# Kernel optimization log

Measured on AMD Instinct MI355X. Metric: run time of the kernel, lower is better.

Reference implementation:

```python
import jax, jax.numpy as jnp
import numpy as np
import math
from jax import lax

B, T, IN_DIM, D, H, L, OUT = 2, 2048, 128, 512, 8, 4, 128
HD = D // H
FF = int(4.0 * D)
NEG = -1e30  # stands in for -inf in the causal mask (identical softmax result)


def setup_inputs() -> dict:
    key = jax.random.key(0)
    ks = jax.random.split(key, 8)
    s = 0.02
    def p(k, shape):
        return jax.random.normal(k, shape, jnp.float32) * s
    return {
        "x": jax.random.normal(ks[0], (B, T, IN_DIM), jnp.float32),
        "Win": p(ks[1], (IN_DIM, D)), "bin_": jnp.zeros((D,), jnp.float32),
        "Wqkv": p(ks[2], (L, D, 3 * D)), "bqkv": jnp.zeros((L, 3 * D), jnp.float32),
        "Wo": p(ks[3], (L, D, D)), "bo": jnp.zeros((L, D), jnp.float32),
        "ln1_g": jnp.ones((L, D), jnp.float32), "ln1_b": jnp.zeros((L, D), jnp.float32),
        "Wf1": p(ks[4], (L, D, FF)), "bf1": jnp.zeros((L, FF), jnp.float32),
        "Wf2": p(ks[5], (L, FF, D)), "bf2": jnp.zeros((L, D), jnp.float32),
        "ln2_g": jnp.ones((L, D), jnp.float32), "ln2_b": jnp.zeros((L, D), jnp.float32),
        "lnf_g": jnp.ones((D,), jnp.float32), "lnf_b": jnp.zeros((D,), jnp.float32),
        "Wout": p(ks[6], (D, OUT)), "bout": jnp.zeros((OUT,), jnp.float32),
    }


def _layernorm(x, g, b, eps=1e-5):
    mu = jnp.mean(x, axis=-1, keepdims=True)
    var = jnp.mean(jnp.square(x - mu), axis=-1, keepdims=True)
    return (x - mu) * lax.rsqrt(var + eps) * g + b


def _sinusoidal_pe(t, d):
    pos = jnp.arange(t, dtype=jnp.float32)[:, None]
    div = jnp.exp(jnp.arange(0, d, 2, dtype=jnp.float32) * (-math.log(10000.0) / d))
    pe = jnp.zeros((t, d), jnp.float32)
    pe = pe.at[:, 0::2].set(jnp.sin(pos * div)).at[:, 1::2].set(jnp.cos(pos * div))
    return pe


def _alibi_bias():
    # ALiBi slopes (H=8 is a power of 2): start = 2**(-2**(-(log2(H)-3)))
    start = 2.0 ** (-(2.0 ** (-(math.log2(H) - 3.0))))
    slopes = jnp.array([start * (start ** i) for i in range(H)], jnp.float32)
    pos = jnp.arange(T)
    dist = jnp.triu(pos[None, :] - pos[:, None]).astype(jnp.float32)  # faithful: .triu() zeroes j<i
    bias = slopes[:, None, None] * dist  # [H,T,T]
    causal = jnp.triu(jnp.ones((T, T), bool), 1)
    return jnp.where(causal[None], NEG, bias)


def _forward(x, Win, bin_, Wqkv, bqkv, Wo, bo, ln1_g, ln1_b, Wf1, bf1, Wf2, bf2,
             ln2_g, ln2_b, lnf_g, lnf_b, Wout, bout):
    x = x @ Win + bin_                      # [B,T,D] project_in
    x = x + _sinusoidal_pe(T, D)            # internal time embedding
    bias = _alibi_bias()                    # [H,T,T]
    scale = 1.0 / math.sqrt(HD)

    def block(h, params):
        wqkv, bq, wo, bo_, g1, b1, wf1, bf1_, wf2, bf2_, g2, b2 = params
        y = _layernorm(h, g1, b1)
        qkv = y @ wqkv + bq                 # [B,T,3D]
        q, k, v = jnp.split(qkv, 3, axis=-1)
        def heads(t):
            return t.reshape(B, T, H, HD).transpose(0, 2, 1, 3)  # [B,H,T,HD]
        q, k, v = heads(q), heads(k), heads(v)
        logits = jnp.einsum('bhqd,bhkd->bhqk', q, k) * scale + bias[None]
        attn = jax.nn.softmax(logits, axis=-1)
        y = jnp.einsum('bhqk,bhkd->bhqd', attn, v)
        y = y.transpose(0, 2, 1, 3).reshape(B, T, D)
        h = h + (y @ wo + bo_)
        y = _layernorm(h, g2, b2)
        y = jax.nn.gelu(y @ wf1 + bf1_, approximate=False) @ wf2 + bf2_
        h = h + y
        return h, None

    x, _ = lax.scan(block, x, (Wqkv, bqkv, Wo, bo, ln1_g, ln1_b, Wf1, bf1, Wf2, bf2, ln2_g, ln2_b))
    x = _layernorm(x, lnf_g, lnf_b)         # final_norm
    return x @ Wout + bout                  # output head


def reference(x, Win, bin_, Wqkv, bqkv, Wo, bo, ln1_g, ln1_b, Wf1, bf1, Wf2, bf2,
              ln2_g, ln2_b, lnf_g, lnf_b, Wout, bout):
    return _forward(x, Win, bin_, Wqkv, bqkv, Wo, bo, ln1_g, ln1_b, Wf1, bf1,
                    Wf2, bf2, ln2_g, ln2_b, lnf_g, lnf_b, Wout, bout)
```

## Files before the change

kernel.cpp:

```cpp
#include <hip/hip_runtime.h>
#include <math.h>
#include <type_traits>
#include <utility>

#define TT 2048
typedef unsigned short u16;
typedef unsigned int u32;
typedef float f32x4 __attribute__((ext_vector_type(4)));
typedef float f32x16 __attribute__((ext_vector_type(16)));
typedef short s16x8 __attribute__((ext_vector_type(8)));
typedef __bf16 bf16x8 __attribute__((ext_vector_type(8)));
typedef __bf16 bf16x2 __attribute__((ext_vector_type(2)));
typedef u32 u32x4 __attribute__((ext_vector_type(4)));

#define L2E8 0.1803368801111731f
#define EXP2(x) __builtin_amdgcn_exp2f(x)

enum { EPI_PE = 0, EPI_QKV = 1, EPI_RES = 2, EPI_GELU = 3, EPI_OUTF = 4 };

template<typename V, typename = void> struct mfma32_takes : std::false_type {};
template<typename V> struct mfma32_takes<V, std::void_t<decltype(
    __builtin_amdgcn_mfma_f32_32x32x16_bf16(std::declval<V>(), std::declval<V>(),
                                            std::declval<f32x16>(), 0, 0, 0))>>
    : std::true_type {};

template<typename VA>
__device__ __forceinline__ f32x16 MFMA32(VA a, VA b, f32x16 c) {
    if constexpr (mfma32_takes<VA>::value) {
        return __builtin_amdgcn_mfma_f32_32x32x16_bf16(a, b, c, 0, 0, 0);
    } else {
        return __builtin_amdgcn_mfma_f32_32x32x16_bf16(
            __builtin_bit_cast(bf16x8, a), __builtin_bit_cast(bf16x8, b), c, 0, 0, 0);
    }
}

__device__ __forceinline__ u16 f2b(float f) {
    u32 u = __float_as_uint(f);
    return (u16)((u + 0x7FFFu + ((u >> 16) & 1u)) >> 16);
}

__device__ __forceinline__ u32 pkbf(float a, float b) {
    bf16x2 t; t[0] = (__bf16)a; t[1] = (__bf16)b;
    return __builtin_bit_cast(u32, t);
}

__device__ __forceinline__ void gload16(const void* g, void* lds_base, int lds_byte_off) {
    __builtin_amdgcn_global_load_lds(
        (const __attribute__((address_space(1))) void*)g,
        (__attribute__((address_space(3))) void*)((char*)lds_base + lds_byte_off),
        16, 0, 0);
}

template<int EPI, int TM, int TN>
__global__ __launch_bounds__(256)
void k_gemm_mfma(const u16* __restrict__ A, const u16* __restrict__ Bt,
                 const float* __restrict__ bias, const float* __restrict__ Rf,
                 void* __restrict__ Cout, u16* __restrict__ Kfp,
                 u16* __restrict__ Vfp, int M, int N, int K)
{
    constexpr int MF = TM / 64;
    constexpr int NF = TN / 64;
    __shared__ __attribute__((aligned(16))) u16 SMEM[TM * 64 + TN * 64];
    u16* As = SMEM;
    u16* Bs = SMEM + TM * 64;
    const int tid = threadIdx.x;
    const int l = tid & 63, wv = tid >> 6;
    const int l31 = l & 31, hi = l >> 5;
    const int wr = wv >> 1, wc = wv & 1;
    const int row0 = blockIdx.y * TM, col0 = blockIdx.x * TN;

    f32x16 acc[MF][NF] = {};

    for (int kt = 0; kt < K; kt += 64) {
#pragma unroll
        for (int i = 0; i < TM / 32; ++i) {
            const int u = i * 256 + wv * 64 + l;
            const int ar = u >> 3, ac = u & 7;
            const int sc = (ac ^ (ar & 7)) << 3;
            const int off = __builtin_amdgcn_readfirstlane((i * 256 + wv * 64) * 16);
            gload16(A + (size_t)(row0 + ar) * K + kt + sc, As, off);
        }
#pragma unroll
        for (int i = 0; i < TN / 32; ++i) {
            const int u = i * 256 + wv * 64 + l;
            const int ar = u >> 3, ac = u & 7;
            const int sc = (ac ^ (ar & 7)) << 3;
            const int off = __builtin_amdgcn_readfirstlane((i * 256 + wv * 64) * 16);
            gload16(Bt + (size_t)(col0 + ar) * K + kt + sc, Bs, off);
        }
        __syncthreads();
        s16x8 af[MF][4], bf[NF][4];
#pragma unroll
        for (int m = 0; m < MF; ++m) {
            const int r = wr * (TM / 2) + m * 32 + l31;
#pragma unroll
            for (int kk = 0; kk < 4; ++kk)
                af[m][kk] = *(const s16x8*)(As + r * 64 + (((kk * 2 + hi) ^ (r & 7)) << 3));
        }
#pragma unroll
        for (int n = 0; n < NF; ++n) {
            const int r = wc * (TN / 2) + n * 32 + l31;
#pragma unroll
            for (int kk = 0; kk < 4; ++kk)
                bf[n][kk] = *(const s16x8*)(Bs + r * 64 + (((kk * 2 + hi) ^ (r & 7)) << 3));
        }
#pragma unroll
        for (int kk = 0; kk < 4; ++kk)
#pragma unroll
            for (int m = 0; m < MF; ++m)
#pragma unroll
                for (int n = 0; n < NF; ++n)
                    acc[m][n] = MFMA32(af[m][kk], bf[n][kk], acc[m][n]);
        __syncthreads();
    }

    if constexpr (EPI == EPI_QKV) {
        if (col0 < 512) {
#pragma unroll
            for (int m = 0; m < MF; ++m)
#pragma unroll
                for (int r = 0; r < 16; ++r) {
                    const int row = row0 + wr * (TM / 2) + m * 32 + (r & 3) + 8 * (r >> 2) + 4 * hi;
#pragma unroll
                    for (int n = 0; n < NF; ++n) {
                        const int col = col0 + wc * (TN / 2) + n * 32 + l31;
                        ((u16*)Cout)[(size_t)row * N + col] = f2b(acc[m][n][r] + bias[col]);
                    }
                }
        } else if (col0 < 1024) {
#pragma unroll
            for (int m = 0; m < MF; ++m)
#pragma unroll
                for (int r = 0; r < 16; ++r) {
                    const int row = row0 + wr * (TM / 2) + m * 32 + (r & 3) + 8 * (r >> 2) + 4 * hi;
                    const int t = row & (TT - 1), bb = row >> 11;
#pragma unroll
                    for (int n = 0; n < NF; ++n) {
                        const int col = col0 + wc * (TN / 2) + n * 32 + l31;
                        const int dd = col - 512;
                        const int hh = dd >> 6, c = (dd >> 3) & 7, j = dd & 7;
                        Kfp[(((size_t)(bb * 8 + hh) * 8 + c) * 2048 + t) * 8 + j]
                            = f2b(acc[m][n][r] + bias[col]);
                    }
                }
        } else {
            u16* TV = SMEM;
#pragma unroll
            for (int m = 0; m < MF; ++m)
#pragma unroll
                for (int r = 0; r < 16; ++r) {
                    const int rr = wr * (TM / 2) + m * 32 + (r & 3) + 8 * (r >> 2) + 4 * hi;
#pragma unroll
                    for (int n = 0; n < NF; ++n) {
                        const int cc_ = wc * (TN / 2) + n * 32 + l31;
                        TV[rr * 128 + cc_] = f2b(acc[m][n][r] + bias[col0 + cc_]);
                    }
                }
            __syncthreads();
            const int gt = (row0 & (TT - 1)) >> 6, bb = row0 >> 11;
            const int hh0 = (col0 - 1024) >> 6;
#pragma unroll
            for (int i = 0; i < 4; ++i) {
                const int u = i * 256 + tid;
                const int hsel = u >> 9, rem = u & 511;
                const int cc = rem >> 6, d = rem & 63;
                u32 pk[4];
#pragma unroll
                for (int jp = 0; jp < 4; ++jp)
                    pk[jp] = (u32)TV[(cc * 8 + 2 * jp) * 128 + hsel * 64 + d]
                           | ((u32)TV[(cc * 8 + 2 * jp + 1) * 128 + hsel * 64 + d] << 16);
                *(uint4*)(Vfp + ((((size_t)(bb * 8 + hh0 + hsel) * 32 + gt) * 8 + cc) * 64 + d) * 8)
                    = make_uint4(pk[0], pk[1], pk[2], pk[3]);
            }
        }
        return;
    }

#pragma unroll
    for (int m = 0; m < MF; ++m)
#pragma unroll
        for (int r = 0; r < 16; ++r) {
            const int row = row0 + wr * (TM / 2) + m * 32 + (r & 3) + 8 * (r >> 2) + 4 * hi;
#pragma unroll
            for (int n = 0; n < NF; ++n) {
                const int col = col0 + wc * (TN / 2) + n * 32 + l31;
                float v = acc[m][n][r] + bias[col];
                const size_t idx = (size_t)row * N + col;
                if constexpr (EPI == EPI_PE) {
                    const int t = row & (TT - 1);
                    const float freq = __expf(-(float)(col & ~1) * 0.017988946039015984f);
                    const float ang = (float)t * freq;
                    v += (col & 1) ? cosf(ang) : sinf(ang);
                    ((float*)Cout)[idx] = v;
                } else if constexpr (EPI == EPI_GELU) {
                    v = 0.5f * v * (1.f + erff(v * 0.7071067811865475f));
                    ((u16*)Cout)[idx] = f2b(v);
                } else if constexpr (EPI == EPI_RES) {
                    ((float*)Cout)[idx] = Rf[idx] + v;
                } else {
                    ((float*)Cout)[idx] = v;
                }
            }
        }
}

__global__ __launch_bounds__(256)
void k_ln(const float* __restrict__ X, const float* __restrict__ g,
          const float* __restrict__ b, u16* __restrict__ Y)
{
    const int lane = threadIdx.x & 63;
    const int row = blockIdx.x * 4 + (threadIdx.x >> 6);
    const float* x = X + (size_t)row * 512 + lane * 8;

    float4 v0 = *(const float4*)x;
    float4 v1 = *(const float4*)(x + 4);
    float vals[8] = {v0.x, v0.y, v0.z, v0.w, v1.x, v1.y, v1.z, v1.w};

    float s = 0.f;
#pragma unroll
    for (int i = 0; i < 8; ++i) s += vals[i];
#pragma unroll
    for (int off = 32; off >= 1; off >>= 1) s += __shfl_xor(s, off);
    const float mu = s * (1.f / 512.f);

    float sq = 0.f;
#pragma unroll
    for (int i = 0; i < 8; ++i) { float d = vals[i] - mu; sq += d * d; }
#pragma unroll
    for (int off = 32; off >= 1; off >>= 1) sq += __shfl_xor(sq, off);
    const float rs = rsqrtf(sq * (1.f / 512.f) + 1e-5f);

    const float* gp = g + lane * 8;
    const float* bp = b + lane * 8;
    float4 g0 = *(const float4*)gp, g1 = *(const float4*)(gp + 4);
    float4 b0 = *(const float4*)bp, b1 = *(const float4*)(bp + 4);
    float ga[8] = {g0.x, g0.y, g0.z, g0.w, g1.x, g1.y, g1.z, g1.w};
    float bb[8] = {b0.x, b0.y, b0.z, b0.w, b1.x, b1.y, b1.z, b1.w};

    u32 pk[4];
#pragma unroll
    for (int i = 0; i < 4; ++i) {
        float a0 = (vals[2 * i]     - mu) * rs * ga[2 * i]     + bb[2 * i];
        float a1 = (vals[2 * i + 1] - mu) * rs * ga[2 * i + 1] + bb[2 * i + 1];
        pk[i] = (u32)f2b(a0) | ((u32)f2b(a1) << 16);
    }
    *(uint4*)(Y + (size_t)row * 512 + lane * 8) = make_uint4(pk[0], pk[1], pk[2], pk[3]);
}

__global__ __launch_bounds__(256, 4)
void k_attn(const u16* __restrict__ qkv, const u16* __restrict__ Kf,
            const u16* __restrict__ Vf, u16* __restrict__ y)
{
    __shared__ float Om[4][32 * 65];
    __shared__ float Ml[4][32][2];
    const int tid = threadIdx.x;
    const int l = tid & 63, w = tid >> 6;
    const int l31 = l & 31, hi = l >> 5;
    const int bx = blockIdx.x;
    const int xcd = bx & 7, s = bx >> 3;
    const int bh = xcd * 2 + (s & 1);
    const int t_tile = 63 - (s >> 1);
    const int b = bh >> 3, hh = bh & 7;
    const int bT = b * TT, hh64 = hh * 64;

    const int qg = t_tile * 32 + l31;
    const int NT = (t_tile >> 1) + 1;

    f32x16 o[2] = {};
    float m = -1e30f, lsum = 0.f;

    if (w < NT) {
        s16x8 qf[4];
        {
            const u16* qsrc = qkv + (size_t)(bT + qg) * 1536 + hh64 + hi * 8;
#pragma unroll
            for (int dk = 0; dk < 4; ++dk) qf[dk] = *(const s16x8*)(qsrc + dk * 16);
        }
        const u16* kfb = Kf + ((size_t)bh * 8 + hi) * 2048 * 8;
        const u16* vfb = Vf + (((size_t)bh * 32) * 8 + hi) * 64 * 8;

        for (int g = w; g < NT; g += 4) {
            s16x8 kf[8];
#pragma unroll
            for (int nb = 0; nb < 2; ++nb)
#pragma unroll
                for (int dk = 0; dk < 4; ++dk)
                    kf[nb * 4 + dk] = *(const s16x8*)(
                        kfb + ((size_t)(dk * 2) * 2048 + g * 64 + nb * 32 + l31) * 8);

            f32x16 sA[2];
            __builtin_amdgcn_s_setprio(1);
#pragma unroll
            for (int nb = 0; nb < 2; ++nb) {
                f32x16 acc = {};
#pragma unroll
                for (int dk = 0; dk < 4; ++dk) acc = MFMA32(kf[nb * 4 + dk], qf[dk], acc);
                sA[nb] = acc;
            }
            __builtin_amdgcn_s_setprio(0);

            if (g == NT - 1) {
                const int kvb = g * 64, hi4 = hi * 4;
#pragma unroll
                for (int nb = 0; nb < 2; ++nb)
#pragma unroll
                    for (int r = 0; r < 16; ++r) {
                        const int kv = kvb + nb * 32 + (r & 3) + 8 * (r >> 2) + hi4;
                        sA[nb][r] = (kv > qg) ? -1e30f : sA[nb][r];
                    }
            }

            float tmp[16];
#pragma unroll
            for (int r = 0; r < 16; ++r) tmp[r] = fmaxf(sA[0][r], sA[1][r]);
#pragma unroll
            for (int st = 8; st >= 1; st >>= 1)
#pragma unroll
                for (int r = 0; r < 8; ++r)
                    if (r < st) tmp[r] = fmaxf(tmp[r], tmp[r + st]);
            float mt = fmaxf(tmp[0], __shfl_xor(tmp[0], 32));
            const bool grow = !__all(mt <= m);
            if (grow) {
                const float mn = fmaxf(m, mt);
                const float alpha = EXP2((m - mn) * L2E8);
                m = mn;
                lsum *= alpha;
#pragma unroll
                for (int dt = 0; dt < 2; ++dt)
#pragma unroll
                    for (int r = 0; r < 16; ++r) o[dt][r] *= alpha;
            }
            const float mc = -m * L2E8;

            float p[2][16];
            float sum[16];
#pragma unroll
            for (int r = 0; r < 16; ++r) {
                p[0][r] = EXP2(fmaf(sA[0][r], L2E8, mc));
                p[1][r] = EXP2(fmaf(sA[1][r], L2E8, mc));
                sum[r] = p[0][r] + p[1][r];
            }
#pragma unroll
            for (int st = 8; st >= 1; st >>= 1)
#pragma unroll
                for (int r = 0; r < 8; ++r)
                    if (r < st) sum[r] += sum[r + st];
            float psum = sum[0] + __shfl_xor(sum[0], 32);
            lsum += psum;

            u32 pk2[2][8], sw2[2][8];
#pragma unroll
            for (int nb = 0; nb < 2; ++nb)
#pragma unroll
                for (int i = 0; i < 8; ++i) {
                    pk2[nb][i] = pkbf(p[nb][2 * i], p[nb][2 * i + 1]);
                    sw2[nb][i] = __shfl_xor(pk2[nb][i], 32);
                }
            s16x8 pa[4];
#pragma unroll
            for (int nb = 0; nb < 2; ++nb)
#pragma unroll
                for (int k16 = 0; k16 < 2; ++k16) {
                    const int i0 = k16 * 4;
                    u32 w0 = hi ? sw2[nb][i0 + 2] : pk2[nb][i0 + 0];
                    u32 w1 = hi ? sw2[nb][i0 + 3] : pk2[nb][i0 + 1];
                    u32 w2 = hi ? pk2[nb][i0 + 2] : sw2[nb][i0 + 0];
                    u32 w3 = hi ? pk2[nb][i0 + 3] : sw2[nb][i0 + 1];
                    u32x4 t4 = {w0, w1, w2, w3};
                    pa[nb * 2 + k16] = __builtin_bit_cast(s16x8, t4);
                }

            __builtin_amdgcn_s_setprio(1);
#pragma unroll
            for (int dt = 0; dt < 2; ++dt) {
                f32x16 acc = o[dt];
#pragma unroll
                for (int ks = 0; ks < 4; ++ks)
                    acc = MFMA32(*(const s16x8*)(
                        vfb + (((size_t)g * 8 + ks * 2) * 64 + dt * 32 + l31) * 8),
                        pa[ks], acc);
                o[dt] = acc;
            }
            __builtin_amdgcn_s_setprio(0);
        }
    }

#pragma unroll
    for (int dt = 0; dt < 2; ++dt)
#pragma unroll
        for (int r = 0; r < 16; ++r) {
            const int d = dt * 32 + (r & 3) + 8 * (r >> 2) + 4 * hi;
            Om[w][l31 * 65 + d] = o[dt][r];
        }
    Ml[w][l31][0] = m;
    Ml[w][l31][1] = lsum;
    __syncthreads();

    const int q = tid & 31, d0 = (tid >> 5) * 8;
    float m0 = Ml[0][q][0], m1 = Ml[1][q][0], m2 = Ml[2][q][0], m3 = Ml[3][q][0];
    const float mstar = fmaxf(fmaxf(m0, m1), fmaxf(m2, m3));
    float sc[4];
    sc[0] = EXP2((m0 - mstar) * L2E8);
    sc[1] = EXP2((m1 - mstar) * L2E8);
    sc[2] = EXP2((m2 - mstar) * L2E8);
    sc[3] = EXP2((m3 - mstar) * L2E8);
    const float lstar = sc[0] * Ml[0][q][1] + sc[1] * Ml[1][q][1]
                      + sc[2] * Ml[2][q][1] + sc[3] * Ml[3][q][1];
    float ov[8];
#pragma unroll
    for (int j = 0; j < 8; ++j) ov[j] = 0.f;
#pragma unroll
    for (int ww = 0; ww < 4; ++ww) {
        const float scw = sc[ww];
        const float* src = &Om[ww][q * 65 + d0];
#pragma unroll
        for (int j = 0; j < 8; ++j) ov[j] = fmaf(scw, src[j], ov[j]);
    }
    const float inv = 1.f / lstar;
    u32 pk[4];
#pragma unroll
    for (int i = 0; i < 4; ++i) pk[i] = pkbf(ov[2 * i] * inv, ov[2 * i + 1] * inv);
    u16* yp = y + (size_t)(bT + t_tile * 32 + q) * 512 + hh64 + d0;
    *(uint4*)yp = make_uint4(pk[0], pk[1], pk[2], pk[3]);
}

__global__ __launch_bounds__(256)
void k_wt_all(const float* __restrict__ Wqkv, const float* __restrict__ Wo,
              const float* __restrict__ Wf1, const float* __restrict__ Wf2,
              const float* __restrict__ Win, const float* __restrict__ Wout,
              u16* __restrict__ WqkvT, u16* __restrict__ WoT,
              u16* __restrict__ Wf1T, u16* __restrict__ Wf2T,
              u16* __restrict__ WinT, u16* __restrict__ WoutT)
{
    __shared__ float T[64][65];
    const int tid = threadIdx.x;
    int id = blockIdx.x;
    const float* W; u16* Wt; int K, N;
    if (id < 3072) {
        const int lyr = id / 768, sub = id - lyr * 768;
        if (sub < 192)      { W = Wqkv + (size_t)lyr * 512 * 1536; Wt = WqkvT + (size_t)lyr * 512 * 1536; K = 512;  N = 1536; id = sub; }
        else if (sub < 256) { W = Wo   + (size_t)lyr * 512 * 512;  Wt = WoT   + (size_t)lyr * 512 * 512;  K = 512;  N = 512;  id = sub - 192; }
        else if (sub < 512) { W = Wf1  + (size_t)lyr * 512 * 2048; Wt = Wf1T  + (size_t)lyr * 512 * 2048; K = 512;  N = 2048; id = sub - 256; }
        else                { W = Wf2  + (size_t)lyr * 2048 * 512; Wt = Wf2T  + (size_t)lyr * 2048 * 512; K = 2048; N = 512;  id = sub - 512; }
    } else if (id < 3088)   { W = Win;  Wt = WinT;  K = 128; N = 512; id -= 3072; }
    else                    { W = Wout; Wt = WoutT; K = 512; N = 128; id -= 3088; }
    const int nt = N >> 6;
    const int ktile = id / nt, ntile = id - ktile * nt;
    const int kb = ktile * 64, nb = ntile * 64;
#pragma unroll
    for (int i = 0; i < 4; ++i) {
        const int r = i * 16 + (tid >> 4), c = (tid & 15) * 4;
        const float4 v = *(const float4*)&W[(size_t)(kb + r) * N + nb + c];
        T[r][c] = v.x; T[r][c + 1] = v.y; T[r][c + 2] = v.z; T[r][c + 3] = v.w;
    }
    __syncthreads();
    const int n = tid >> 2, k0 = (tid & 3) * 16;
    u32 pk[8];
#pragma unroll
    for (int i = 0; i < 8; ++i)
        pk[i] = pkbf(T[k0 + 2 * i][n], T[k0 + 2 * i + 1][n]);
    uint4* dst = (uint4*)(Wt + (size_t)(nb + n) * K + kb + k0);
    dst[0] = make_uint4(pk[0], pk[1], pk[2], pk[3]);
    dst[1] = make_uint4(pk[4], pk[5], pk[6], pk[7]);
}

__global__ __launch_bounds__(256)
void k_f2b(const float* __restrict__ x, u16* __restrict__ xb)
{
    const int g = blockIdx.x * 256 + threadIdx.x;
    const float4* s = (const float4*)(x + (size_t)g * 8);
    float4 a = s[0], c = s[1];
    u32 pk[4] = {
        (u32)f2b(a.x) | ((u32)f2b(a.y) << 16), (u32)f2b(a.z) | ((u32)f2b(a.w) << 16),
        (u32)f2b(c.x) | ((u32)f2b(c.y) << 16), (u32)f2b(c.z) | ((u32)f2b(c.w) << 16)};
    *(uint4*)(xb + (size_t)g * 8) = make_uint4(pk[0], pk[1], pk[2], pk[3]);
}

extern "C" void kernel_launch(void* const* d_in, const int* in_sizes, int n_in,
                              void* d_out, int out_size, void* d_ws, size_t ws_size,
                              hipStream_t stream)
{
    const float* x    = (const float*)d_in[0];
    const float* Win  = (const float*)d_in[1];
    const float* bin_ = (const float*)d_in[2];
    const float* Wqkv = (const float*)d_in[3];
    const float* bqkv = (const float*)d_in[4];
    const float* Wo   = (const float*)d_in[5];
    const float* bo   = (const float*)d_in[6];
    const float* ln1g = (const float*)d_in[7];
    const float* ln1b = (const float*)d_in[8];
    const float* Wf1  = (const float*)d_in[9];
    const float* bf1  = (const float*)d_in[10];
    const float* Wf2  = (const float*)d_in[11];
    const float* bf2  = (const float*)d_in[12];
    const float* ln2g = (const float*)d_in[13];
    const float* ln2b = (const float*)d_in[14];
    const float* lnfg = (const float*)d_in[15];
    const float* lnfb = (const float*)d_in[16];
    const float* Wout = (const float*)d_in[17];
    const float* bout = (const float*)d_in[18];
    float* out = (float*)d_out;

    const int M = 4096;
    char* ws = (char*)d_ws;
    float* h    = (float*)(ws + 0);
    u16*   y    = (u16*)(ws + 8388608);
    u16*   big  = (u16*)(ws + 12582912);
    u16*   Kf   = (u16*)(ws + 29360128);
    u16*   Vf   = (u16*)(ws + 33554432);
    u16*   xb   = big;
    u16*   WinT  = (u16*)(ws + 37748736);
    u16*   WoutT = (u16*)(ws + 37879808);
    u16*   WqkvT = (u16*)(ws + 38010880);
    u16*   WoT   = (u16*)(ws + 44302336);
    u16*   Wf1T  = (u16*)(ws + 46399488);
    u16*   Wf2T  = (u16*)(ws + 54788096);

    dim3 blk(256);

    k_f2b<<<256, blk, 0, stream>>>(x, xb);
    k_wt_all<<<3104, blk, 0, stream>>>(Wqkv, Wo, Wf1, Wf2, Win, Wout,
                                       WqkvT, WoT, Wf1T, Wf2T, WinT, WoutT);

    k_gemm_mfma<EPI_PE, 64, 64><<<dim3(8, 64), blk, 0, stream>>>(
        xb, WinT, bin_, nullptr, h, nullptr, nullptr, M, 512, 128);

    for (int lyr = 0; lyr < 4; ++lyr) {
        k_ln<<<1024, blk, 0, stream>>>(h, ln1g + lyr * 512, ln1b + lyr * 512, y);
        k_gemm_mfma<EPI_QKV, 64, 128><<<dim3(12, 64), blk, 0, stream>>>(
            y, WqkvT + (size_t)lyr * 512 * 1536, bqkv + lyr * 1536, nullptr,
            big, Kf, Vf, M, 1536, 512);
        k_attn<<<1024, blk, 0, stream>>>(big, Kf, Vf, y);
        k_gemm_mfma<EPI_RES, 64, 64><<<dim3(8, 64), blk, 0, stream>>>(
            y, WoT + (size_t)lyr * 512 * 512, bo + lyr * 512, h, h, nullptr, nullptr, M, 512, 512);
        k_ln<<<1024, blk, 0, stream>>>(h, ln2g + lyr * 512, ln2b + lyr * 512, y);
        k_gemm_mfma<EPI_GELU, 64, 128><<<dim3(16, 64), blk, 0, stream>>>(
            y, Wf1T + (size_t)lyr * 512 * 2048, bf1 + lyr * 2048, nullptr,
            big, nullptr, nullptr, M, 2048, 512);
        k_gemm_mfma<EPI_RES, 64, 64><<<dim3(8, 64), blk, 0, stream>>>(
            big, Wf2T + (size_t)lyr * 2048 * 512, bf2 + lyr * 512, h, h, nullptr, nullptr, M, 512, 2048);
    }

    k_ln<<<1024, blk, 0, stream>>>(h, lnfg, lnfb, y);
    k_gemm_mfma<EPI_OUTF, 64, 64><<<dim3(2, 64), blk, 0, stream>>>(
        y, WoutT, bout, nullptr, out, nullptr, nullptr, M, 128, 512);
}
```

Before: 434.9 us.

## Fuse LayerNorm into the A-operand load of following GEMMs

Removes the standalone LayerNorm kernels and instead has each consuming GEMM compute per-row mean and rstd from the fp32 residual, then normalize and pack to bf16 while staging the A tile into LDS. This drops nine kernel launches and the bf16 round-trip of the normalized activations through global memory. In exchange, every column block of the GEMM reloads and re-reduces the fp32 rows, the A path loses the async global_load_lds, and variance switches to E[x^2]-mu^2, which is less numerically stable.

```diff
diff --git a/kernel.cpp b/kernel.cpp
--- a/kernel.cpp
+++ b/kernel.cpp
@@ -51,9 +51,11 @@
         16, 0, 0);
 }
 
-template<int EPI, int TM, int TN>
+template<int EPI, int TM, int TN, int LNA>
 __global__ __launch_bounds__(256)
-void k_gemm_mfma(const u16* __restrict__ A, const u16* __restrict__ Bt,
+void k_gemm_mfma(const u16* __restrict__ A, const float* __restrict__ hA,
+                 const float* __restrict__ lnG, const float* __restrict__ lnB,
+                 const u16* __restrict__ Bt,
                  const float* __restrict__ bias, const float* __restrict__ Rf,
                  void* __restrict__ Cout, u16* __restrict__ Kfp,
                  u16* __restrict__ Vfp, int M, int N, int K)
@@ -61,6 +63,10 @@
     constexpr int MF = TM / 64;
     constexpr int NF = TN / 64;
     __shared__ __attribute__((aligned(16))) u16 SMEM[TM * 64 + TN * 64];
+    __shared__ float Gs[LNA ? 512 : 1];
+    __shared__ float Bsh[LNA ? 512 : 1];
+    __shared__ float Mu[LNA ? 64 : 1];
+    __shared__ float Rs[LNA ? 64 : 1];
     u16* As = SMEM;
     u16* Bs = SMEM + TM * 64;
     const int tid = threadIdx.x;
@@ -69,16 +75,66 @@
     const int wr = wv >> 1, wc = wv & 1;
     const int row0 = blockIdx.y * TM, col0 = blockIdx.x * TN;
 
+    if constexpr (LNA) {
+        if (tid < 128) ((float4*)Gs)[tid] = ((const float4*)lnG)[tid];
+        else           ((float4*)Bsh)[tid - 128] = ((const float4*)lnB)[tid - 128];
+        const int r_ = tid >> 2, q_ = tid & 3;
+        const float* hp = hA + (size_t)(row0 + r_) * 512 + q_ * 128;
+        float s_ = 0.f, sq_ = 0.f;
+#pragma unroll
+        for (int i = 0; i < 32; ++i) {
+            float4 v = ((const float4*)hp)[i];
+            s_  += v.x + v.y + v.z + v.w;
+            sq_ += v.x * v.x + v.y * v.y + v.z * v.z + v.w * v.w;
+        }
+        s_  += __shfl_xor(s_, 1);  s_  += __shfl_xor(s_, 2);
+        sq_ += __shfl_xor(sq_, 1); sq_ += __shfl_xor(sq_, 2);
+        if (q_ == 0) {
+            const float muv = s_ * (1.f / 512.f);
+            Mu[r_] = muv;
+            Rs[r_] = rsqrtf(sq_ * (1.f / 512.f) - muv * muv + 1e-5f);
+        }
+        __syncthreads();
+    }
+
     f32x16 acc[MF][NF] = {};
 
     for (int kt = 0; kt < K; kt += 64) {
-#pragma unroll
-        for (int i = 0; i < TM / 32; ++i) {
-            const int u = i * 256 + wv * 64 + l;
-            const int ar = u >> 3, ac = u & 7;
-            const int sc = (ac ^ (ar & 7)) << 3;
-            const int off = __builtin_amdgcn_readfirstlane((i * 256 + wv * 64) * 16);
-            gload16(A + (size_t)(row0 + ar) * K + kt + sc, As, off);
+        if constexpr (LNA) {
+#pragma unroll
+            for (int i = 0; i < TM / 32; ++i) {
+                const int u = i * 256 + wv * 64 + l;
+                const int ar = u >> 3, ac = u & 7;
+                const int sc = (ac ^ (ar & 7)) << 3;
+                const float* hp = hA + (size_t)(row0 + ar) * 512 + kt + sc;
+                float4 a0 = *(const float4*)hp;
+                float4 a1 = *(const float4*)(hp + 4);
+                const float muv = Mu[ar], rsv = Rs[ar];
+                const float* gp = Gs + kt + sc;
+                const float* bp2 = Bsh + kt + sc;
+                float4 g0 = *(const float4*)gp, g1 = *(const float4*)(gp + 4);
+                float4 b0 = *(const float4*)bp2, b1 = *(const float4*)(bp2 + 4);
+                float av[8] = {a0.x, a0.y, a0.z, a0.w, a1.x, a1.y, a1.z, a1.w};
+                float gv[8] = {g0.x, g0.y, g0.z, g0.w, g1.x, g1.y, g1.z, g1.w};
+                float bv[8] = {b0.x, b0.y, b0.z, b0.w, b1.x, b1.y, b1.z, b1.w};
+                u32 pk[4];
+#pragma unroll
+                for (int j = 0; j < 4; ++j) {
+                    float e0 = (av[2*j]   - muv) * rsv * gv[2*j]   + bv[2*j];
+                    float e1 = (av[2*j+1] - muv) * rsv * gv[2*j+1] + bv[2*j+1];
+                    pk[j] = pkbf(e0, e1);
+                }
+                *(uint4*)(As + ar * 64 + (ac << 3)) = make_uint4(pk[0], pk[1], pk[2], pk[3]);
+            }
+        } else {
+#pragma unroll
+            for (int i = 0; i < TM / 32; ++i) {
+                const int u = i * 256 + wv * 64 + l;
+                const int ar = u >> 3, ac = u & 7;
+                const int sc = (ac ^ (ar & 7)) << 3;
+                const int off = __builtin_amdgcn_readfirstlane((i * 256 + wv * 64) * 16);
+                gload16(A + (size_t)(row0 + ar) * K + kt + sc, As, off);
+            }
         }
 #pragma unroll
         for (int i = 0; i < TN / 32; ++i) {
@@ -202,49 +258,6 @@
                 }
             }
         }
-}
-
-__global__ __launch_bounds__(256)
-void k_ln(const float* __restrict__ X, const float* __restrict__ g,
-          const float* __restrict__ b, u16* __restrict__ Y)
-{
-    const int lane = threadIdx.x & 63;
-    const int row = blockIdx.x * 4 + (threadIdx.x >> 6);
-    const float* x = X + (size_t)row * 512 + lane * 8;
-
-    float4 v0 = *(const float4*)x;
-    float4 v1 = *(const float4*)(x + 4);
-    float vals[8] = {v0.x, v0.y, v0.z, v0.w, v1.x, v1.y, v1.z, v1.w};
-
-    float s = 0.f;
-#pragma unroll
-    for (int i = 0; i < 8; ++i) s += vals[i];
-#pragma unroll
-    for (int off = 32; off >= 1; off >>= 1) s += __shfl_xor(s, off);
-    const float mu = s * (1.f / 512.f);
-
-    float sq = 0.f;
-#pragma unroll
-    for (int i = 0; i < 8; ++i) { float d = vals[i] - mu; sq += d * d; }
-#pragma unroll
-    for (int off = 32; off >= 1; off >>= 1) sq += __shfl_xor(sq, off);
-    const float rs = rsqrtf(sq * (1.f / 512.f) + 1e-5f);
-
-    const float* gp = g + lane * 8;
-    const float* bp = b + lane * 8;
-    float4 g0 = *(const float4*)gp, g1 = *(const float4*)(gp + 4);
-    float4 b0 = *(const float4*)bp, b1 = *(const float4*)(bp + 4);
-    float ga[8] = {g0.x, g0.y, g0.z, g0.w, g1.x, g1.y, g1.z, g1.w};
-    float bb[8] = {b0.x, b0.y, b0.z, b0.w, b1.x, b1.y, b1.z, b1.w};
-
-    u32 pk[4];
-#pragma unroll
-    for (int i = 0; i < 4; ++i) {
-        float a0 = (vals[2 * i]     - mu) * rs * ga[2 * i]     + bb[2 * i];
-        float a1 = (vals[2 * i + 1] - mu) * rs * ga[2 * i + 1] + bb[2 * i + 1];
-        pk[i] = (u32)f2b(a0) | ((u32)f2b(a1) << 16);
-    }
-    *(uint4*)(Y + (size_t)row * 512 + lane * 8) = make_uint4(pk[0], pk[1], pk[2], pk[3]);
 }
 
 __global__ __launch_bounds__(256, 4)
@@ -522,26 +535,27 @@
     k_wt_all<<<3104, blk, 0, stream>>>(Wqkv, Wo, Wf1, Wf2, Win, Wout,
                                        WqkvT, WoT, Wf1T, Wf2T, WinT, WoutT);
 
-    k_gemm_mfma<EPI_PE, 64, 64><<<dim3(8, 64), blk, 0, stream>>>(
-        xb, WinT, bin_, nullptr, h, nullptr, nullptr, M, 512, 128);
+    k_gemm_mfma<EPI_PE, 64, 64, 0><<<dim3(8, 64), blk, 0, stream>>>(
+        xb, nullptr, nullptr, nullptr, WinT, bin_, nullptr, h, nullptr, nullptr, M, 512, 128);
 
     for (int lyr = 0; lyr < 4; ++lyr) {
-        k_ln<<<1024, blk, 0, stream>>>(h, ln1g + lyr * 512, ln1b + lyr * 512, y);
-        k_gemm_mfma<EPI_QKV, 64, 128><<<dim3(12, 64), blk, 0, stream>>>(
-            y, WqkvT + (size_t)lyr * 512 * 1536, bqkv + lyr * 1536, nullptr,
+        k_gemm_mfma<EPI_QKV, 64, 128, 1><<<dim3(12, 64), blk, 0, stream>>>(
+            nullptr, h, ln1g + lyr * 512, ln1b + lyr * 512,
+            WqkvT + (size_t)lyr * 512 * 1536, bqkv + lyr * 1536, nullptr,
             big, Kf, Vf, M, 1536, 512);
         k_attn<<<1024, blk, 0, stream>>>(big, Kf, Vf, y);
-        k_gemm_mfma<EPI_RES, 64, 64><<<dim3(8, 64), blk, 0, stream>>>(
-            y, WoT + (size_t)lyr * 512 * 512, bo + lyr * 512, h, h, nullptr, nullptr, M, 512, 512);
-        k_ln<<<1024, blk, 0, stream>>>(h, ln2g + lyr * 512, ln2b + lyr * 512, y);
-        k_gemm_mfma<EPI_GELU, 64, 128><<<dim3(16, 64), blk, 0, stream>>>(
-            y, Wf1T + (size_t)lyr * 512 * 2048, bf1 + lyr * 2048, nullptr,
+        k_gemm_mfma<EPI_RES, 64, 64, 0><<<dim3(8, 64), blk, 0, stream>>>(
+            y, nullptr, nullptr, nullptr,
+            WoT + (size_t)lyr * 512 * 512, bo + lyr * 512, h, h, nullptr, nullptr, M, 512, 512);
+        k_gemm_mfma<EPI_GELU, 64, 128, 1><<<dim3(16, 64), blk, 0, stream>>>(
+            nullptr, h, ln2g + lyr * 512, ln2b + lyr * 512,
+            Wf1T + (size_t)lyr * 512 * 2048, bf1 + lyr * 2048, nullptr,
             big, nullptr, nullptr, M, 2048, 512);
-        k_gemm_mfma<EPI_RES, 64, 64><<<dim3(8, 64), blk, 0, stream>>>(
-            big, Wf2T + (size_t)lyr * 2048 * 512, bf2 + lyr * 512, h, h, nullptr, nullptr, M, 512, 2048);
-    }
-
-    k_ln<<<1024, blk, 0, stream>>>(h, lnfg, lnfb, y);
-    k_gemm_mfma<EPI_OUTF, 64, 64><<<dim3(2, 64), blk, 0, stream>>>(
-        y, WoutT, bout, nullptr, out, nullptr, nullptr, M, 128, 512);
-}
+        k_gemm_mfma<EPI_RES, 64, 64, 0><<<dim3(8, 64), blk, 0, stream>>>(
+            big, nullptr, nullptr, nullptr,
+            Wf2T + (size_t)lyr * 2048 * 512, bf2 + lyr * 512, h, h, nullptr, nullptr, M, 512, 2048);
+    }
+
+    k_gemm_mfma<EPI_OUTF, 64, 64, 1><<<dim3(2, 64), blk, 0, stream>>>(
+        nullptr, h, lnfg, lnfb, WoutT, bout, nullptr, out, nullptr, nullptr, M, 128, 512);
+}
```

New measurement: 544.5 us. +25.2%, slower.
